# Performance work log

Hardware: AMD Instinct MI355X
Metric: run time of the kernel (lower is better)

The kernel has to match this reference:

```python
import jax, jax.numpy as jnp
import numpy as np

NUM_CLASSES = 32
N = 8 * 1024 * 1024  # e.g. batch of 8 segmentation masks at 1024x1024


def setup_inputs() -> dict:
    key = jax.random.key(0)
    k1, k2 = jax.random.split(key)
    y_true = jax.random.randint(k1, (N,), 0, NUM_CLASSES, dtype=jnp.int64 if jax.config.jax_enable_x64 else jnp.int32).astype(jnp.int32)
    y_pred = jax.random.randint(k2, (N,), 0, NUM_CLASSES, dtype=jnp.int32)
    return {"y_true": y_true, "y_pred": y_pred}


def reference(y_true, y_pred):
    # Equivalent to: mask = y_true != 0; cm = one_hot(y_true[mask]).T @ one_hot(y_pred[mask])
    # computed in O(N) via scatter-add on the combined (true, pred) index.
    C = NUM_CLASSES
    yt = y_true.reshape(-1)
    yp = y_pred.reshape(-1)
    w = (yt != 0).astype(jnp.float32)          # masked-out pixels contribute 0
    idx = yt * C + yp                           # combined bin index in [0, C*C)
    cm = jnp.zeros((C * C,), dtype=jnp.float32).at[idx].add(w)
    return cm.reshape(C, C)
```

## Files before the change

### kernel.cpp

```cpp
#include <hip/hip_runtime.h>

#define NUM_CLASSES 32
#define NBINS (NUM_CLASSES * NUM_CLASSES)
#define BLOCK 256
#define GRID1 2048
#define GRID2 64

__global__ __launch_bounds__(BLOCK) void confmat_partial(
    const int* __restrict__ y_true,
    const int* __restrict__ y_pred,
    unsigned int* __restrict__ ws,
    int n)
{
    __shared__ unsigned int hist[NBINS];
    #pragma unroll
    for (int i = threadIdx.x; i < NBINS; i += BLOCK) hist[i] = 0u;
    __syncthreads();

    const int tid    = blockIdx.x * BLOCK + threadIdx.x;
    const int stride = GRID1 * BLOCK;
    const int n4 = n >> 2;
    const int4* __restrict__ t4 = (const int4*)y_true;
    const int4* __restrict__ p4 = (const int4*)y_pred;

    int i = tid;
    for (; i + 3 * stride < n4; i += 4 * stride) {
        int4 a0 = t4[i];              int4 b0 = p4[i];
        int4 a1 = t4[i + stride];     int4 b1 = p4[i + stride];
        int4 a2 = t4[i + 2 * stride]; int4 b2 = p4[i + 2 * stride];
        int4 a3 = t4[i + 3 * stride]; int4 b3 = p4[i + 3 * stride];
        if (a0.x) atomicAdd(&hist[a0.x * NUM_CLASSES + b0.x], 1u);
        if (a0.y) atomicAdd(&hist[a0.y * NUM_CLASSES + b0.y], 1u);
        if (a0.z) atomicAdd(&hist[a0.z * NUM_CLASSES + b0.z], 1u);
        if (a0.w) atomicAdd(&hist[a0.w * NUM_CLASSES + b0.w], 1u);
        if (a1.x) atomicAdd(&hist[a1.x * NUM_CLASSES + b1.x], 1u);
        if (a1.y) atomicAdd(&hist[a1.y * NUM_CLASSES + b1.y], 1u);
        if (a1.z) atomicAdd(&hist[a1.z * NUM_CLASSES + b1.z], 1u);
        if (a1.w) atomicAdd(&hist[a1.w * NUM_CLASSES + b1.w], 1u);
        if (a2.x) atomicAdd(&hist[a2.x * NUM_CLASSES + b2.x], 1u);
        if (a2.y) atomicAdd(&hist[a2.y * NUM_CLASSES + b2.y], 1u);
        if (a2.z) atomicAdd(&hist[a2.z * NUM_CLASSES + b2.z], 1u);
        if (a2.w) atomicAdd(&hist[a2.w * NUM_CLASSES + b2.w], 1u);
        if (a3.x) atomicAdd(&hist[a3.x * NUM_CLASSES + b3.x], 1u);
        if (a3.y) atomicAdd(&hist[a3.y * NUM_CLASSES + b3.y], 1u);
        if (a3.z) atomicAdd(&hist[a3.z * NUM_CLASSES + b3.z], 1u);
        if (a3.w) atomicAdd(&hist[a3.w * NUM_CLASSES + b3.w], 1u);
    }
    for (; i < n4; i += stride) {
        int4 a = t4[i]; int4 b = p4[i];
        if (a.x) atomicAdd(&hist[a.x * NUM_CLASSES + b.x], 1u);
        if (a.y) atomicAdd(&hist[a.y * NUM_CLASSES + b.y], 1u);
        if (a.z) atomicAdd(&hist[a.z * NUM_CLASSES + b.z], 1u);
        if (a.w) atomicAdd(&hist[a.w * NUM_CLASSES + b.w], 1u);
    }
    for (int j = (n4 << 2) + tid; j < n; j += stride) {
        int a = y_true[j]; int b = y_pred[j];
        if (a) atomicAdd(&hist[a * NUM_CLASSES + b], 1u);
    }

    __syncthreads();

    uint4* __restrict__ w4 = (uint4*)(ws + (size_t)blockIdx.x * NBINS);
    const uint4* __restrict__ h4 = (const uint4*)hist;
    w4[threadIdx.x] = h4[threadIdx.x];
}

__global__ __launch_bounds__(BLOCK) void confmat_reduce(
    const unsigned int* __restrict__ ws,
    float* __restrict__ out)
{
    const int t = threadIdx.x;
    const int pbase = blockIdx.x * (GRID1 / GRID2);
    const uint4* __restrict__ w4 = (const uint4*)ws;
    unsigned int sx = 0, sy = 0, sz = 0, sw = 0;
    #pragma unroll 8
    for (int p = 0; p < GRID1 / GRID2; ++p) {
        uint4 v = w4[(size_t)(pbase + p) * (NBINS / 4) + t];
        sx += v.x; sy += v.y; sz += v.z; sw += v.w;
    }
    atomicAdd(&out[4 * t + 0], (float)sx);
    atomicAdd(&out[4 * t + 1], (float)sy);
    atomicAdd(&out[4 * t + 2], (float)sz);
    atomicAdd(&out[4 * t + 3], (float)sw);
}

extern "C" void kernel_launch(void* const* d_in, const int* in_sizes, int n_in,
                              void* d_out, int out_size, void* d_ws, size_t ws_size,
                              hipStream_t stream) {
    const int* y_true = (const int*)d_in[0];
    const int* y_pred = (const int*)d_in[1];
    float* out = (float*)d_out;
    unsigned int* ws = (unsigned int*)d_ws;
    int n = in_sizes[0];

    hipMemsetAsync(out, 0, (size_t)out_size * sizeof(float), stream);

    confmat_partial<<<GRID1, BLOCK, 0, stream>>>(y_true, y_pred, ws, n);
    confmat_reduce<<<GRID2, BLOCK, 0, stream>>>(ws, out);
}
```

Before: 102.0 us.

## Drop mask branches, zero row 0 in reduce, remove memset

The histogram loop no longer branches on y_true being zero. Those pixels are counted into row 0, and the reduce kernel zeroes that row when it writes the output. The reduce is reorganised so each of 32 blocks owns one confusion-matrix row. Each block sums the partial histograms through a shared-memory atomic stage and stores the result directly, so the memset and the global float atomics are no longer needed. The bin index uses shift/or instead of multiply/add, which assumes labels stay in [0,32).

```diff
diff --git a/kernel.cpp b/kernel.cpp
--- a/kernel.cpp
+++ b/kernel.cpp
@@ -4,7 +4,7 @@
 #define NBINS (NUM_CLASSES * NUM_CLASSES)
 #define BLOCK 256
 #define GRID1 2048
-#define GRID2 64
+#define GRID2 NUM_CLASSES
 
 __global__ __launch_bounds__(BLOCK) void confmat_partial(
     const int* __restrict__ y_true,
@@ -29,33 +29,32 @@
         int4 a1 = t4[i + stride];     int4 b1 = p4[i + stride];
         int4 a2 = t4[i + 2 * stride]; int4 b2 = p4[i + 2 * stride];
         int4 a3 = t4[i + 3 * stride]; int4 b3 = p4[i + 3 * stride];
-        if (a0.x) atomicAdd(&hist[a0.x * NUM_CLASSES + b0.x], 1u);
-        if (a0.y) atomicAdd(&hist[a0.y * NUM_CLASSES + b0.y], 1u);
-        if (a0.z) atomicAdd(&hist[a0.z * NUM_CLASSES + b0.z], 1u);
-        if (a0.w) atomicAdd(&hist[a0.w * NUM_CLASSES + b0.w], 1u);
-        if (a1.x) atomicAdd(&hist[a1.x * NUM_CLASSES + b1.x], 1u);
-        if (a1.y) atomicAdd(&hist[a1.y * NUM_CLASSES + b1.y], 1u);
-        if (a1.z) atomicAdd(&hist[a1.z * NUM_CLASSES + b1.z], 1u);
-        if (a1.w) atomicAdd(&hist[a1.w * NUM_CLASSES + b1.w], 1u);
-        if (a2.x) atomicAdd(&hist[a2.x * NUM_CLASSES + b2.x], 1u);
-        if (a2.y) atomicAdd(&hist[a2.y * NUM_CLASSES + b2.y], 1u);
-        if (a2.z) atomicAdd(&hist[a2.z * NUM_CLASSES + b2.z], 1u);
-        if (a2.w) atomicAdd(&hist[a2.w * NUM_CLASSES + b2.w], 1u);
-        if (a3.x) atomicAdd(&hist[a3.x * NUM_CLASSES + b3.x], 1u);
-        if (a3.y) atomicAdd(&hist[a3.y * NUM_CLASSES + b3.y], 1u);
-        if (a3.z) atomicAdd(&hist[a3.z * NUM_CLASSES + b3.z], 1u);
-        if (a3.w) atomicAdd(&hist[a3.w * NUM_CLASSES + b3.w], 1u);
+        atomicAdd(&hist[(a0.x << 5) | b0.x], 1u);
+        atomicAdd(&hist[(a0.y << 5) | b0.y], 1u);
+        atomicAdd(&hist[(a0.z << 5) | b0.z], 1u);
+        atomicAdd(&hist[(a0.w << 5) | b0.w], 1u);
+        atomicAdd(&hist[(a1.x << 5) | b1.x], 1u);
+        atomicAdd(&hist[(a1.y << 5) | b1.y], 1u);
+        atomicAdd(&hist[(a1.z << 5) | b1.z], 1u);
+        atomicAdd(&hist[(a1.w << 5) | b1.w], 1u);
+        atomicAdd(&hist[(a2.x << 5) | b2.x], 1u);
+        atomicAdd(&hist[(a2.y << 5) | b2.y], 1u);
+        atomicAdd(&hist[(a2.z << 5) | b2.z], 1u);
+        atomicAdd(&hist[(a2.w << 5) | b2.w], 1u);
+        atomicAdd(&hist[(a3.x << 5) | b3.x], 1u);
+        atomicAdd(&hist[(a3.y << 5) | b3.y], 1u);
+        atomicAdd(&hist[(a3.z << 5) | b3.z], 1u);
+        atomicAdd(&hist[(a3.w << 5) | b3.w], 1u);
     }
     for (; i < n4; i += stride) {
         int4 a = t4[i]; int4 b = p4[i];
-        if (a.x) atomicAdd(&hist[a.x * NUM_CLASSES + b.x], 1u);
-        if (a.y) atomicAdd(&hist[a.y * NUM_CLASSES + b.y], 1u);
-        if (a.z) atomicAdd(&hist[a.z * NUM_CLASSES + b.z], 1u);
-        if (a.w) atomicAdd(&hist[a.w * NUM_CLASSES + b.w], 1u);
+        atomicAdd(&hist[(a.x << 5) | b.x], 1u);
+        atomicAdd(&hist[(a.y << 5) | b.y], 1u);
+        atomicAdd(&hist[(a.z << 5) | b.z], 1u);
+        atomicAdd(&hist[(a.w << 5) | b.w], 1u);
     }
     for (int j = (n4 << 2) + tid; j < n; j += stride) {
-        int a = y_true[j]; int b = y_pred[j];
-        if (a) atomicAdd(&hist[a * NUM_CLASSES + b], 1u);
+        atomicAdd(&hist[(y_true[j] << 5) | y_pred[j]], 1u);
     }
 
     __syncthreads();
@@ -69,19 +68,33 @@
     const unsigned int* __restrict__ ws,
     float* __restrict__ out)
 {
-    const int t = threadIdx.x;
-    const int pbase = blockIdx.x * (GRID1 / GRID2);
+    __shared__ unsigned int sums[NUM_CLASSES];
+    if (threadIdx.x < NUM_CLASSES) sums[threadIdx.x] = 0u;
+    __syncthreads();
+
+    const int q = threadIdx.x & 7;
+    const int c = threadIdx.x >> 3;
+    const int row4 = blockIdx.x * (NUM_CLASSES / 4);
     const uint4* __restrict__ w4 = (const uint4*)ws;
+
     unsigned int sx = 0, sy = 0, sz = 0, sw = 0;
+    const int chunk = GRID1 / 32;
     #pragma unroll 8
-    for (int p = 0; p < GRID1 / GRID2; ++p) {
-        uint4 v = w4[(size_t)(pbase + p) * (NBINS / 4) + t];
+    for (int k = 0; k < chunk; ++k) {
+        int p = c * chunk + k;
+        uint4 v = w4[(size_t)p * (NBINS / 4) + row4 + q];
         sx += v.x; sy += v.y; sz += v.z; sw += v.w;
     }
-    atomicAdd(&out[4 * t + 0], (float)sx);
-    atomicAdd(&out[4 * t + 1], (float)sy);
-    atomicAdd(&out[4 * t + 2], (float)sz);
-    atomicAdd(&out[4 * t + 3], (float)sw);
+    atomicAdd(&sums[q * 4 + 0], sx);
+    atomicAdd(&sums[q * 4 + 1], sy);
+    atomicAdd(&sums[q * 4 + 2], sz);
+    atomicAdd(&sums[q * 4 + 3], sw);
+    __syncthreads();
+
+    if (threadIdx.x < NUM_CLASSES) {
+        float v = (blockIdx.x == 0) ? 0.0f : (float)sums[threadIdx.x];
+        out[blockIdx.x * NUM_CLASSES + threadIdx.x] = v;
+    }
 }
 
 extern "C" void kernel_launch(void* const* d_in, const int* in_sizes, int n_in,
@@ -93,8 +106,6 @@
     unsigned int* ws = (unsigned int*)d_ws;
     int n = in_sizes[0];
 
-    hipMemsetAsync(out, 0, (size_t)out_size * sizeof(float), stream);
-
     confmat_partial<<<GRID1, BLOCK, 0, stream>>>(y_true, y_pred, ws, n);
     confmat_reduce<<<GRID2, BLOCK, 0, stream>>>(ws, out);
 }
```

Result: no change. 101.2 us (-0.8%).
